# Performance work log

Measured on AMD Instinct MI355X. Metric: run time of the kernel, lower is better.

## Reference

```python
import jax, jax.numpy as jnp
import numpy as np

HID = 512
EMB = 768
TOP_K = 8
LN_EPS = 1e-5
NORM_EPS = 1e-12


def _mlp_ln(x, W1, b1, W2, b2, g, beta):
    # Linear -> ReLU -> Linear -> LayerNorm
    h = jax.nn.relu(x @ W1 + b1)
    h = h @ W2 + b2
    mu = jnp.mean(h, axis=-1, keepdims=True)
    var = jnp.var(h, axis=-1, keepdims=True)
    return (h - mu) * jax.lax.rsqrt(var + LN_EPS) * g + beta


def _l2norm(x):
    n = jnp.linalg.norm(x, axis=-1, keepdims=True)
    return x / jnp.maximum(n, NORM_EPS)


def setup_inputs() -> dict:
    key = jax.random.key(0)
    ks = jax.random.split(key, 12)
    s_in = 1.0 / np.sqrt(EMB)
    s_h = 1.0 / np.sqrt(HID)
    inp = {
        "query_embeddings": jax.random.normal(ks[0], (64, 32, EMB), jnp.float32),
        "doc_embeddings": jax.random.normal(ks[1], (50000, 16, EMB), jnp.float32),
        "qW1": jax.random.normal(ks[2], (EMB, HID), jnp.float32) * s_in,
        "qb1": jnp.zeros((HID,), jnp.float32),
        "qW2": jax.random.normal(ks[3], (HID, HID), jnp.float32) * s_h,
        "qb2": jnp.zeros((HID,), jnp.float32),
        "qg": jnp.ones((HID,), jnp.float32),
        "qbeta": jnp.zeros((HID,), jnp.float32),
        "dW1": jax.random.normal(ks[4], (EMB, HID), jnp.float32) * s_in,
        "db1": jnp.zeros((HID,), jnp.float32),
        "dW2": jax.random.normal(ks[5], (HID, HID), jnp.float32) * s_h,
        "db2": jnp.zeros((HID,), jnp.float32),
        "dg": jnp.ones((HID,), jnp.float32),
        "dbeta": jnp.zeros((HID,), jnp.float32),
        "pW": jax.random.normal(ks[6], (HID, HID), jnp.float32) * s_h,
        "pb": jnp.zeros((HID,), jnp.float32),
        "temperature": jnp.asarray(1.0, jnp.float32),
    }
    return inp


def reference(query_embeddings, doc_embeddings, qW1, qb1, qW2, qb2, qg, qbeta,
              dW1, db1, dW2, db2, dg, dbeta, pW, pb, temperature):
    # Mean-pool over token dims, encode with MLP+LayerNorm
    q_repr = _mlp_ln(query_embeddings.mean(axis=1), qW1, qb1, qW2, qb2, qg, qbeta)  # [B,H]
    d_repr = _mlp_ln(doc_embeddings.mean(axis=1), dW1, db1, dW2, db2, dg, dbeta)    # [N,H]
    q_norm = _l2norm(q_repr @ pW + pb)
    d_norm = _l2norm(d_repr @ pW + pb)
    scores = (q_norm @ d_norm.T) / temperature  # [B,N]
    top_k_scores, top_k_indices = jax.lax.top_k(scores, TOP_K)  # [B,K]
    retrieved_docs = doc_embeddings[top_k_indices]  # [B,K,doc_len,EMB]
    return top_k_scores, retrieved_docs
```

## Files before the change

### kernel.cpp

```cpp
#include <hip/hip_runtime.h>

#define NQ 64
#define ND 50000
#define NDP 50048
#define MT (NDP + NQ)
#define QTOK 32
#define DTOK 16
#define EMB 768
#define HID 512

typedef short s16x8 __attribute__((ext_vector_type(8)));
typedef float f32x4 __attribute__((ext_vector_type(4)));

__device__ __forceinline__ unsigned short f2bf(float f) {
    union { float f; unsigned u; } x; x.f = f;
    unsigned r = x.u + 0x7fffu + ((x.u >> 16) & 1u);
    return (unsigned short)(r >> 16);
}
__device__ __forceinline__ float bf2f(unsigned short h) {
    union { unsigned u; float f; } x; x.u = ((unsigned)h) << 16;
    return x.f;
}
__device__ __forceinline__ unsigned packhi2(float a, float b) {
    return (unsigned)f2bf(a) | ((unsigned)f2bf(b) << 16);
}
__device__ __forceinline__ unsigned packlo2(float a, float b) {
    unsigned short ha = f2bf(a), hb = f2bf(b);
    return (unsigned)f2bf(a - bf2f(ha)) | ((unsigned)f2bf(b - bf2f(hb)) << 16);
}

__device__ __forceinline__ void gload_lds16(const void* g, void* l) {
    __builtin_amdgcn_global_load_lds(
        (const __attribute__((address_space(1))) void*)g,
        (__attribute__((address_space(3))) void*)l, 16, 0, 0);
}


__global__ void pool_aug_all(const float* __restrict__ de, const float* __restrict__ qe,
                             ushort* __restrict__ out) {
    int blk = blockIdx.x, t = threadIdx.x;
    const float* src;
    int T;
    size_t orow;
    if (blk < ND) { src = de + (size_t)blk * DTOK * EMB; T = DTOK; orow = blk; }
    else          { int qr = blk - ND; src = qe + (size_t)qr * QTOK * EMB; T = QTOK; orow = NDP + qr; }
    const float4* ip = (const float4*)src + t;
    float4 a = make_float4(0.f, 0.f, 0.f, 0.f);
    for (int i = 0; i < T; ++i) {
        float4 v = ip[(size_t)i * (EMB / 4)];
        a.x += v.x; a.y += v.y; a.z += v.z; a.w += v.w;
    }
    const float s = 1.0f / (float)T;
    float v0 = a.x * s, v1 = a.y * s, v2 = a.z * s, v3 = a.w * s;
    ushort* base = out + orow * (2 * EMB);
    *(uint2*)(base + t * 4)       = make_uint2(packhi2(v0, v1), packhi2(v2, v3));
    *(uint2*)(base + EMB + t * 4) = make_uint2(packlo2(v0, v1), packlo2(v2, v3));
}

__global__ void wconv_all(const float* __restrict__ dW1, const float* __restrict__ qW1,
                          const float* __restrict__ dW2, const float* __restrict__ qW2,
                          const float* __restrict__ pW,
                          const float* __restrict__ dg, const float* __restrict__ qg,
                          ushort* __restrict__ W1p, ushort* __restrict__ QW1p,
                          ushort* __restrict__ W2p, ushort* __restrict__ QW2p,
                          ushort* __restrict__ W3d, ushort* __restrict__ W3q) {
    int n = blockIdx.x, seg = blockIdx.y;
    const float* W; const float* scale = nullptr; ushort* o; int K;
    switch (seg) {
        case 0:  W = dW1; o = W1p;  K = EMB; break;
        case 1:  W = qW1; o = QW1p; K = EMB; break;
        case 2:  W = dW2; o = W2p;  K = HID; break;
        case 3:  W = qW2; o = QW2p; K = HID; break;
        case 4:  W = pW;  o = W3d;  K = HID; scale = dg; break;
        default: W = pW;  o = W3q;  K = HID; scale = qg; break;
    }
    ushort* base = o + (size_t)n * 2 * K;
    for (int k = threadIdx.x; k < K; k += blockDim.x) {
        float v = W[(size_t)k * HID + n];
        if (scale) v *= scale[k];
        unsigned short hi = f2bf(v);
        base[k]     = hi;
        base[K + k] = f2bf(v - bf2f(hi));
    }
}

__global__ void uv_prep(const float* __restrict__ pW, const float* __restrict__ pb,
                        const float* __restrict__ dg, const float* __restrict__ dbe,
                        const float* __restrict__ qg, const float* __restrict__ qbe,
                        float* __restrict__ ud, float* __restrict__ vvd,
                        float* __restrict__ uq, float* __restrict__ vvq) {
    int n = blockIdx.x;
    float a = 0.f, b = 0.f, c = 0.f, d = 0.f;
    for (int k = threadIdx.x; k < HID; k += 256) {
        float w = pW[(size_t)k * HID + n];
        a += dg[k] * w; b += dbe[k] * w; c += qg[k] * w; d += qbe[k] * w;
    }
    #pragma unroll
    for (int o = 32; o > 0; o >>= 1) {
        a += __shfl_xor(a, o); b += __shfl_xor(b, o);
        c += __shfl_xor(c, o); d += __shfl_xor(d, o);
    }
    __shared__ float red[4][4];
    int wv = threadIdx.x >> 6, ln = threadIdx.x & 63;
    if (ln == 0) { red[wv][0] = a; red[wv][1] = b; red[wv][2] = c; red[wv][3] = d; }
    __syncthreads();
    if (threadIdx.x == 0) {
        float A = 0, B = 0, C = 0, D = 0;
        #pragma unroll
        for (int i = 0; i < 4; ++i) { A += red[i][0]; B += red[i][1]; C += red[i][2]; D += red[i][3]; }
        ud[n] = A; vvd[n] = B + pb[n]; uq[n] = C; vvq[n] = D + pb[n];
    }
}

template <int MODE>
__global__ __launch_bounds__(512, 4) void mfma_gemm2(const ushort* __restrict__ A,
                                                     const ushort* __restrict__ Bd,
                                                     const ushort* __restrict__ Bq,
                                                     const float* __restrict__ pard,
                                                     const float* __restrict__ parq,
                                                     const float* __restrict__ auxd,
                                                     const float* __restrict__ auxq,
                                                     const float2* __restrict__ statsIn,
                                                     float2* __restrict__ sumsOut,
                                                     float* __restrict__ normpOut,
                                                     void* __restrict__ out,
                                                     int M, int K) {
    __shared__ ushort As[128 * 64];
    __shared__ ushort Bs[256 * 64];
    __shared__ float redS[4][128];
    __shared__ float redQ[4][128];
    const int Ks = 2 * K;
    const int bm = blockIdx.x * 128;
    const int bn = blockIdx.y * 256;
    const bool isq = (bm >= NDP);
    const ushort* B = isq ? Bq : Bd;
    const int tid = threadIdx.x;
    const int lane = tid & 63;
    const int wave = tid >> 6;
    const int wr = wave >> 2;
    const int wc = wave & 3;
    f32x4 acc[4][4] = {};

    for (int k0 = 0; k0 < 3 * K; k0 += 64) {
        const int ka = (k0 < 2 * K) ? k0 : k0 - 2 * K;
        const int kb = (k0 < K) ? k0 : k0 - K;
        #pragma unroll
        for (int c = 0; c < 2; ++c) {
            int idx = c * 512 + tid;
            int row = idx >> 3, s = idx & 7;
            int gr = bm + row; if (gr >= M) gr = M - 1;
            int ks = (s ^ (row & 7)) << 3;
            gload_lds16(A + (size_t)gr * Ks + ka + ks, As + idx * 8);
        }
        #pragma unroll
        for (int c = 0; c < 4; ++c) {
            int idx = c * 512 + tid;
            int n = idx >> 3, s = idx & 7;
            int ks = (s ^ (n & 7)) << 3;
            gload_lds16(B + (size_t)(bn + n) * Ks + kb + ks, Bs + idx * 8);
        }
        __syncthreads();

        #pragma unroll
        for (int kk = 0; kk < 2; ++kk) {
            const int sp = kk * 4 + (lane >> 4);
            s16x8 a[4], b[4];
            #pragma unroll
            for (int i = 0; i < 4; ++i) {
                int r = wr * 64 + i * 16 + (lane & 15);
                a[i] = *(const s16x8*)(As + r * 64 + ((sp ^ (r & 7)) << 3));
            }
            #pragma unroll
            for (int j = 0; j < 4; ++j) {
                int n = wc * 64 + j * 16 + (lane & 15);
                b[j] = *(const s16x8*)(Bs + n * 64 + ((sp ^ (n & 7)) << 3));
            }
            #pragma unroll
            for (int i = 0; i < 4; ++i)
                #pragma unroll
                for (int j = 0; j < 4; ++j)
                    acc[i][j] = __builtin_amdgcn_mfma_f32_16x16x32_bf16(a[i], b[j], acc[i][j], 0, 0, 0);
        }
        __syncthreads();
    }

    if (MODE == 1 || MODE == 2) {
        const float* bias = isq ? parq : pard;
        float bv[4];
        #pragma unroll
        for (int j = 0; j < 4; ++j) bv[j] = bias[bn + wc * 64 + j * 16 + (lane & 15)];

        if (MODE == 2) {
            #pragma unroll
            for (int i = 0; i < 4; ++i)
                #pragma unroll
                for (int r = 0; r < 4; ++r) {
                    float ps = 0.f, pq = 0.f;
                    #pragma unroll
                    for (int j = 0; j < 4; ++j) {
                        float v = acc[i][j][r] + bv[j];
                        ps += v; pq += v * v;
                    }
                    #pragma unroll
                    for (int o = 1; o < 16; o <<= 1) { ps += __shfl_xor(ps, o); pq += __shfl_xor(pq, o); }
                    if ((lane & 15) == 0) {
                        int rl = wr * 64 + i * 16 + ((lane >> 4) << 2) + r;
                        redS[wc][rl] = ps; redQ[wc][rl] = pq;
                    }
                }
            __syncthreads();
            if (tid < 128) {
                float s = redS[0][tid] + redS[1][tid] + redS[2][tid] + redS[3][tid];
                float q = redQ[0][tid] + redQ[1][tid] + redQ[2][tid] + redQ[3][tid];
                int grow = bm + tid;
                if (grow < M) sumsOut[(size_t)grow * 2 + blockIdx.y] = make_float2(s, q);
            }
        }

        #pragma unroll
        for (int j = 0; j < 4; ++j) {
            int col = bn + wc * 64 + j * 16 + (lane & 15);
            #pragma unroll
            for (int i = 0; i < 4; ++i)
                #pragma unroll
                for (int r = 0; r < 4; ++r) {
                    int grow = bm + wr * 64 + i * 16 + ((lane >> 4) << 2) + r;
                    if (grow >= M) continue;
                    float v = acc[i][j][r] + bv[j];
                    if (MODE == 1) v = fmaxf(v, 0.0f);
                    unsigned short hi = f2bf(v);
                    ushort* op = (ushort*)out + (size_t)grow * (2 * HID);
                    op[col]       = hi;
                    op[HID + col] = f2bf(v - bf2f(hi));
                }
        }
    } else {
        const float* u  = isq ? parq : pard;
        const float* vv = isq ? auxq : auxd;
        float uj[4], vj[4];
        #pragma unroll
        for (int j = 0; j < 4; ++j) {
            int col = bn + wc * 64 + j * 16 + (lane & 15);
            uj[j] = u[col]; vj[j] = vv[col];
        }
        #pragma unroll
        for (int i = 0; i < 4; ++i)
            #pragma unroll
            for (int r = 0; r < 4; ++r) {
                int grow = bm + wr * 64 + i * 16 + ((lane >> 4) << 2) + r;
                int gsr  = grow < M ? grow : M - 1;
                float2 p0 = statsIn[(size_t)gsr * 2 + 0];
                float2 p1 = statsIn[(size_t)gsr * 2 + 1];
                float s  = p0.x + p1.x, qq = p0.y + p1.y;
                float mu  = s * (1.0f / 512.0f);
                float var = qq * (1.0f / 512.0f) - mu * mu;
                float rs  = rsqrtf(var + 1e-5f);
                float ps = 0.f;
                #pragma unroll
                for (int j = 0; j < 4; ++j) {
                    float val = rs * (acc[i][j][r] - mu * uj[j]) + vj[j];
                    ps += val * val;
                    if (grow < M) {
                        int col = bn + wc * 64 + j * 16 + (lane & 15);
                        unsigned short hi = f2bf(val);
                        ushort* op = (ushort*)out + (size_t)grow * (2 * HID);
                        op[col]       = hi;
                        op[HID + col] = f2bf(val - bf2f(hi));
                    }
                }
                #pragma unroll
                for (int o = 1; o < 16; o <<= 1) ps += __shfl_xor(ps, o);
                if ((lane & 15) == 0) {
                    int rl = wr * 64 + i * 16 + ((lane >> 4) << 2) + r;
                    redS[wc][rl] = ps;
                }
            }
        __syncthreads();
        if (tid < 128) {
            float s = redS[0][tid] + redS[1][tid] + redS[2][tid] + redS[3][tid];
            int grow = bm + tid;
            if (grow < M) normpOut[(size_t)grow * 2 + blockIdx.y] = s;
        }
    }
}

__global__ __launch_bounds__(512, 4) void mfma_scores(const ushort* __restrict__ A,
                                                      const ushort* __restrict__ B,
                                                      const float* __restrict__ normp,
                                                      float* __restrict__ out,
                                                      int M, int N_B, int K, long ldo,
                                                      const float* __restrict__ temp, int rowOff) {
    __shared__ ushort As[128 * 64];
    __shared__ ushort Bs[256 * 64];
    const int Ks = 2 * K;
    const int bm = blockIdx.x * 128;
    const int bn = blockIdx.y * 256;
    const int tid = threadIdx.x;
    const int lane = tid & 63;
    const int wave = tid >> 6;
    const int wr = wave >> 2;
    const int wc = wave & 3;
    f32x4 acc[4][4] = {};

    for (int k0 = 0; k0 < 3 * K; k0 += 64) {
        const int ka = (k0 < 2 * K) ? k0 : k0 - 2 * K;
        const int kb = (k0 < K) ? k0 : k0 - K;
        #pragma unroll
        for (int c = 0; c < 2; ++c) {
            int idx = c * 512 + tid;
            int row = idx >> 3, s = idx & 7;
            int gr = bm + row; if (gr >= M) gr = M - 1;
            int ks = (s ^ (row & 7)) << 3;
            gload_lds16(A + (size_t)gr * Ks + ka + ks, As + idx * 8);
        }
        #pragma unroll
        for (int c = 0; c < 4; ++c) {
            int idx = c * 512 + tid;
            int n = idx >> 3, s = idx & 7;
            int gn = bn + n; if (gn >= N_B) gn = N_B - 1;
            int ks = (s ^ (n & 7)) << 3;
            gload_lds16(B + (size_t)gn * Ks + kb + ks, Bs + idx * 8);
        }
        __syncthreads();

        #pragma unroll
        for (int kk = 0; kk < 2; ++kk) {
            const int sp = kk * 4 + (lane >> 4);
            s16x8 a[4], b[4];
            #pragma unroll
            for (int i = 0; i < 4; ++i) {
                int r = wr * 64 + i * 16 + (lane & 15);
                a[i] = *(const s16x8*)(As + r * 64 + ((sp ^ (r & 7)) << 3));
            }
            #pragma unroll
            for (int j = 0; j < 4; ++j) {
                int n = wc * 64 + j * 16 + (lane & 15);
                b[j] = *(const s16x8*)(Bs + n * 64 + ((sp ^ (n & 7)) << 3));
            }
            #pragma unroll
            for (int i = 0; i < 4; ++i)
                #pragma unroll
                for (int j = 0; j < 4; ++j)
                    acc[i][j] = __builtin_amdgcn_mfma_f32_16x16x32_bf16(a[i], b[j], acc[i][j], 0, 0, 0);
        }
        __syncthreads();
    }

    float invT = 1.0f / temp[0];
    float rB[4];
    #pragma unroll
    for (int j = 0; j < 4; ++j) {
        int gcol = bn + wc * 64 + j * 16 + (lane & 15);
        int gc = gcol < N_B ? gcol : N_B - 1;
        float n2 = normp[(size_t)gc * 2] + normp[(size_t)gc * 2 + 1];
        rB[j] = 1.0f / fmaxf(sqrtf(n2), 1e-12f);
    }
    #pragma unroll
    for (int i = 0; i < 4; ++i)
        #pragma unroll
        for (int r = 0; r < 4; ++r) {
            int grow = bm + wr * 64 + i * 16 + ((lane >> 4) << 2) + r;
            int gr = grow < M ? grow : M - 1;
            float n2a = normp[(size_t)(rowOff + gr) * 2] + normp[(size_t)(rowOff + gr) * 2 + 1];
            float rA = 1.0f / fmaxf(sqrtf(n2a), 1e-12f);
            #pragma unroll
            for (int j = 0; j < 4; ++j) {
                int gcol = bn + wc * 64 + j * 16 + (lane & 15);
                if (grow < M && gcol < N_B)
                    out[(size_t)grow * ldo + gcol] = acc[i][j][r] * rA * rB[j] * invT;
            }
        }
}

__global__ __launch_bounds__(256) void topk_kernel(const float* __restrict__ scores,
                                                   float* __restrict__ out_scores,
                                                   int* __restrict__ out_idx, int N) {
    __shared__ float ls[2048];
    __shared__ int   li[2048];
    const int q   = blockIdx.x;
    const int tid = threadIdx.x;
    const float* row = scores + (size_t)q * N;
    float s[8]; int ix[8];
    #pragma unroll
    for (int i = 0; i < 8; ++i) { s[i] = -1e30f; ix[i] = 0x7fffffff; }
    for (int j = tid; j < N; j += 256) {
        float v = row[j];
        if (v > s[7]) {
            s[7] = v; ix[7] = j;
            #pragma unroll
            for (int t = 7; t > 0; --t) {
                bool sw = (s[t] > s[t-1]) || (s[t] == s[t-1] && ix[t] < ix[t-1]);
                if (sw) {
                    float tv = s[t]; s[t] = s[t-1]; s[t-1] = tv;
                    int   ti = ix[t]; ix[t] = ix[t-1]; ix[t-1] = ti;
                }
            }
        }
    }
    #pragma unroll
    for (int i = 0; i < 8; ++i) { ls[tid * 8 + i] = s[i]; li[tid * 8 + i] = ix[i]; }
    __syncthreads();
    for (int w = 64; w >= 1; w >>= 2) {
        if (tid < w) {
            #pragma unroll
            for (int i = 0; i < 8; ++i) { s[i] = -1e30f; ix[i] = 0x7fffffff; }
            #pragma unroll
            for (int c = 0; c < 32; ++c) {
                float v  = ls[tid * 32 + c];
                int   vi = li[tid * 32 + c];
                bool better = (v > s[7]) || (v == s[7] && vi < ix[7]);
                if (better) {
                    s[7] = v; ix[7] = vi;
                    #pragma unroll
                    for (int t = 7; t > 0; --t) {
                        bool sw = (s[t] > s[t-1]) || (s[t] == s[t-1] && ix[t] < ix[t-1]);
                        if (sw) {
                            float tv = s[t]; s[t] = s[t-1]; s[t-1] = tv;
                            int   ti = ix[t]; ix[t] = ix[t-1]; ix[t-1] = ti;
                        }
                    }
                }
            }
        }
        __syncthreads();
        if (tid < w) {
            #pragma unroll
            for (int i = 0; i < 8; ++i) { ls[tid * 8 + i] = s[i]; li[tid * 8 + i] = ix[i]; }
        }
        __syncthreads();
    }
    if (tid < 8) {
        out_scores[(size_t)q * 8 + tid] = ls[tid];
        out_idx[q * 8 + tid]            = li[tid];
    }
}

__global__ __launch_bounds__(256) void gather_kernel(const float* __restrict__ docs,
                                                     const int* __restrict__ idx,
                                                     float* __restrict__ out) {
    const int b = blockIdx.x;
    const int d = idx[b];
    const float4* src = (const float4*)(docs + (size_t)d * DTOK * EMB);
    float4*       dst = (float4*)(out + (size_t)b * DTOK * EMB);
    for (int i = threadIdx.x; i < DTOK * EMB / 4; i += 256) dst[i] = src[i];
}

extern "C" void kernel_launch(void* const* d_in, const int* in_sizes, int n_in,
                              void* d_out, int out_size, void* d_ws, size_t ws_size,
                              hipStream_t stream) {
    const float* qe   = (const float*)d_in[0];
    const float* de   = (const float*)d_in[1];
    const float* qW1  = (const float*)d_in[2];
    const float* qb1  = (const float*)d_in[3];
    const float* qW2  = (const float*)d_in[4];
    const float* qb2  = (const float*)d_in[5];
    const float* qg   = (const float*)d_in[6];
    const float* qbe  = (const float*)d_in[7];
    const float* dW1  = (const float*)d_in[8];
    const float* db1  = (const float*)d_in[9];
    const float* dW2  = (const float*)d_in[10];
    const float* db2  = (const float*)d_in[11];
    const float* dg   = (const float*)d_in[12];
    const float* dbe  = (const float*)d_in[13];
    const float* pW   = (const float*)d_in[14];
    const float* pb   = (const float*)d_in[15];
    const float* temp = (const float*)d_in[16];

    float* out = (float*)d_out;

    char* w = (char*)d_ws;
    float*  scores = (float*)w;                 w += (size_t)NQ * ND * 4;
    ushort* W1p    = (ushort*)w;                w += (size_t)HID * 2 * EMB * 2;
    ushort* W2p    = (ushort*)w;                w += (size_t)HID * 2 * HID * 2;
    ushort* W3d    = (ushort*)w;                w += (size_t)HID * 2 * HID * 2;
    ushort* QW1p   = (ushort*)w;                w += (size_t)HID * 2 * EMB * 2;
    ushort* QW2p   = (ushort*)w;                w += (size_t)HID * 2 * HID * 2;
    ushort* W3q    = (ushort*)w;                w += (size_t)HID * 2 * HID * 2;
    float*  ud     = (float*)w;                 w += HID * 4;
    float*  vvd    = (float*)w;                 w += HID * 4;
    float*  uq     = (float*)w;                 w += HID * 4;
    float*  vvq    = (float*)w;                 w += HID * 4;
    float2* sums   = (float2*)w;                w += (size_t)MT * 2 * 8;
    float*  normp  = (float*)w;                 w += (size_t)MT * 2 * 4;
    int*    tidx   = (int*)w;                   w += 4096;
    ushort* pooled = (ushort*)w;                w += (size_t)MT * 2 * EMB * 2;
    ushort* h1a    = (ushort*)w;                w += (size_t)MT * 2 * HID * 2;
    ushort* h2a    = pooled;
    ushort* Daug   = h1a;
    ushort* qaug   = Daug + (size_t)NDP * 2 * HID;

    const int GM = (MT + 127) / 128;

    wconv_all<<<dim3(512, 6), 256, 0, stream>>>(dW1, qW1, dW2, qW2, pW, dg, qg,
                                                W1p, QW1p, W2p, QW2p, W3d, W3q);
    uv_prep<<<512, 256, 0, stream>>>(pW, pb, dg, dbe, qg, qbe, ud, vvd, uq, vvq);

    pool_aug_all<<<ND + NQ, 192, 0, stream>>>(de, qe, pooled);
    mfma_gemm2<1><<<dim3(GM, 2), 512, 0, stream>>>(pooled, W1p, QW1p, db1, qb1,
                                                   nullptr, nullptr, nullptr, nullptr, nullptr,
                                                   h1a, MT, EMB);
    mfma_gemm2<2><<<dim3(GM, 2), 512, 0, stream>>>(h1a, W2p, QW2p, db2, qb2,
                                                   nullptr, nullptr, nullptr, sums, nullptr,
                                                   h2a, MT, HID);
    mfma_gemm2<3><<<dim3(GM, 2), 512, 0, stream>>>(h2a, W3d, W3q, ud, uq,
                                                   vvd, vvq, sums, nullptr, normp,
                                                   Daug, MT, HID);

    mfma_scores<<<dim3(1, (ND + 255) / 256), 512, 0, stream>>>(qaug, Daug, normp, scores,
                                                               NQ, ND, HID, (long)ND, temp, NDP);

    topk_kernel<<<NQ, 256, 0, stream>>>(scores, out, tidx, ND);
    gather_kernel<<<NQ * 8, 256, 0, stream>>>(de, tidx, out + NQ * 8);
}
```

Measured before the change: 1.299 ms.

## Triple-buffer LDS tiles with async prefetch in GEMM and scores kernels

Both MFMA GEMM kernels switch from a single LDS buffer with load-then-sync to a three-slot ring. Tiles are prefetched two K-steps ahead, with explicit vmcnt waits and raw s_barriers in place of __syncthreads. The goal is to overlap global-to-LDS transfers with MFMA compute. LDS use triples to about 144 KB per block and the occupancy hint of 4 is dropped, so fewer blocks can be resident per CU.

```diff
diff --git a/kernel.cpp b/kernel.cpp
--- a/kernel.cpp
+++ b/kernel.cpp
@@ -113,20 +113,20 @@
 }
 
 template <int MODE>
-__global__ __launch_bounds__(512, 4) void mfma_gemm2(const ushort* __restrict__ A,
-                                                     const ushort* __restrict__ Bd,
-                                                     const ushort* __restrict__ Bq,
-                                                     const float* __restrict__ pard,
-                                                     const float* __restrict__ parq,
-                                                     const float* __restrict__ auxd,
-                                                     const float* __restrict__ auxq,
-                                                     const float2* __restrict__ statsIn,
-                                                     float2* __restrict__ sumsOut,
-                                                     float* __restrict__ normpOut,
-                                                     void* __restrict__ out,
-                                                     int M, int K) {
-    __shared__ ushort As[128 * 64];
-    __shared__ ushort Bs[256 * 64];
+__global__ __launch_bounds__(512) void mfma_gemm2(const ushort* __restrict__ A,
+                                                  const ushort* __restrict__ Bd,
+                                                  const ushort* __restrict__ Bq,
+                                                  const float* __restrict__ pard,
+                                                  const float* __restrict__ parq,
+                                                  const float* __restrict__ auxd,
+                                                  const float* __restrict__ auxq,
+                                                  const float2* __restrict__ statsIn,
+                                                  float2* __restrict__ sumsOut,
+                                                  float* __restrict__ normpOut,
+                                                  void* __restrict__ out,
+                                                  int M, int K) {
+    __shared__ ushort As[3][128 * 64];
+    __shared__ ushort Bs[3][256 * 64];
     __shared__ float redS[4][128];
     __shared__ float redQ[4][128];
     const int Ks = 2 * K;
@@ -139,28 +139,47 @@
     const int wave = tid >> 6;
     const int wr = wave >> 2;
     const int wc = wave & 3;
+    const int nt = (3 * K) >> 6;
     f32x4 acc[4][4] = {};
 
-    for (int k0 = 0; k0 < 3 * K; k0 += 64) {
+    auto STAGE = [&](int kt, int slot) {
+        const int k0 = kt << 6;
         const int ka = (k0 < 2 * K) ? k0 : k0 - 2 * K;
         const int kb = (k0 < K) ? k0 : k0 - K;
+        ushort* Asl = &As[slot][0];
+        ushort* Bsl = &Bs[slot][0];
         #pragma unroll
         for (int c = 0; c < 2; ++c) {
             int idx = c * 512 + tid;
             int row = idx >> 3, s = idx & 7;
             int gr = bm + row; if (gr >= M) gr = M - 1;
             int ks = (s ^ (row & 7)) << 3;
-            gload_lds16(A + (size_t)gr * Ks + ka + ks, As + idx * 8);
+            gload_lds16(A + (size_t)gr * Ks + ka + ks, Asl + idx * 8);
         }
         #pragma unroll
         for (int c = 0; c < 4; ++c) {
             int idx = c * 512 + tid;
             int n = idx >> 3, s = idx & 7;
             int ks = (s ^ (n & 7)) << 3;
-            gload_lds16(B + (size_t)(bn + n) * Ks + kb + ks, Bs + idx * 8);
-        }
-        __syncthreads();
-
+            gload_lds16(B + (size_t)(bn + n) * Ks + kb + ks, Bsl + idx * 8);
+        }
+    };
+
+    STAGE(0, 0);
+    STAGE(1, 1);
+    for (int t = 0; t < nt; ++t) {
+        if (t + 2 < nt) {
+            STAGE(t + 2, (t + 2) % 3);
+            asm volatile("s_waitcnt vmcnt(12)" ::: "memory");
+        } else if (t + 1 < nt) {
+            asm volatile("s_waitcnt vmcnt(6)" ::: "memory");
+        } else {
+            asm volatile("s_waitcnt vmcnt(0)" ::: "memory");
+        }
+        __builtin_amdgcn_sched_barrier(0);
+        __builtin_amdgcn_s_barrier();
+        const ushort* Asl = &As[t % 3][0];
+        const ushort* Bsl = &Bs[t % 3][0];
         #pragma unroll
         for (int kk = 0; kk < 2; ++kk) {
             const int sp = kk * 4 + (lane >> 4);
@@ -168,12 +187,12 @@
             #pragma unroll
             for (int i = 0; i < 4; ++i) {
                 int r = wr * 64 + i * 16 + (lane & 15);
-                a[i] = *(const s16x8*)(As + r * 64 + ((sp ^ (r & 7)) << 3));
+                a[i] = *(const s16x8*)(Asl + r * 64 + ((sp ^ (r & 7)) << 3));
             }
             #pragma unroll
             for (int j = 0; j < 4; ++j) {
                 int n = wc * 64 + j * 16 + (lane & 15);
-                b[j] = *(const s16x8*)(Bs + n * 64 + ((sp ^ (n & 7)) << 3));
+                b[j] = *(const s16x8*)(Bsl + n * 64 + ((sp ^ (n & 7)) << 3));
             }
             #pragma unroll
             for (int i = 0; i < 4; ++i)
@@ -181,7 +200,8 @@
                 for (int j = 0; j < 4; ++j)
                     acc[i][j] = __builtin_amdgcn_mfma_f32_16x16x32_bf16(a[i], b[j], acc[i][j], 0, 0, 0);
         }
-        __syncthreads();
+        __builtin_amdgcn_sched_barrier(0);
+        __builtin_amdgcn_s_barrier();
     }
 
     if (MODE == 1 || MODE == 2) {
@@ -284,14 +304,14 @@
     }
 }
 
-__global__ __launch_bounds__(512, 4) void mfma_scores(const ushort* __restrict__ A,
-                                                      const ushort* __restrict__ B,
-                                                      const float* __restrict__ normp,
-                                                      float* __restrict__ out,
-                                                      int M, int N_B, int K, long ldo,
-                                                      const float* __restrict__ temp, int rowOff) {
-    __shared__ ushort As[128 * 64];
-    __shared__ ushort Bs[256 * 64];
+__global__ __launch_bounds__(512) void mfma_scores(const ushort* __restrict__ A,
+                                                   const ushort* __restrict__ B,
+                                                   const float* __restrict__ normp,
+                                                   float* __restrict__ out,
+                                                   int M, int N_B, int K, long ldo,
+                                                   const float* __restrict__ temp, int rowOff) {
+    __shared__ ushort As[3][128 * 64];
+    __shared__ ushort Bs[3][256 * 64];
     const int Ks = 2 * K;
     const int bm = blockIdx.x * 128;
     const int bn = blockIdx.y * 256;
@@ -300,18 +320,22 @@
     const int wave = tid >> 6;
     const int wr = wave >> 2;
     const int wc = wave & 3;
+    const int nt = (3 * K) >> 6;
     f32x4 acc[4][4] = {};
 
-    for (int k0 = 0; k0 < 3 * K; k0 += 64) {
+    auto STAGE = [&](int kt, int slot) {
+        const int k0 = kt << 6;
         const int ka = (k0 < 2 * K) ? k0 : k0 - 2 * K;
         const int kb = (k0 < K) ? k0 : k0 - K;
+        ushort* Asl = &As[slot][0];
+        ushort* Bsl = &Bs[slot][0];
         #pragma unroll
         for (int c = 0; c < 2; ++c) {
             int idx = c * 512 + tid;
             int row = idx >> 3, s = idx & 7;
             int gr = bm + row; if (gr >= M) gr = M - 1;
             int ks = (s ^ (row & 7)) << 3;
-            gload_lds16(A + (size_t)gr * Ks + ka + ks, As + idx * 8);
+            gload_lds16(A + (size_t)gr * Ks + ka + ks, Asl + idx * 8);
         }
         #pragma unroll
         for (int c = 0; c < 4; ++c) {
@@ -319,10 +343,25 @@
             int n = idx >> 3, s = idx & 7;
             int gn = bn + n; if (gn >= N_B) gn = N_B - 1;
             int ks = (s ^ (n & 7)) << 3;
-            gload_lds16(B + (size_t)gn * Ks + kb + ks, Bs + idx * 8);
-        }
-        __syncthreads();
-
+            gload_lds16(B + (size_t)gn * Ks + kb + ks, Bsl + idx * 8);
+        }
+    };
+
+    STAGE(0, 0);
+    STAGE(1, 1);
+    for (int t = 0; t < nt; ++t) {
+        if (t + 2 < nt) {
+            STAGE(t + 2, (t + 2) % 3);
+            asm volatile("s_waitcnt vmcnt(12)" ::: "memory");
+        } else if (t + 1 < nt) {
+            asm volatile("s_waitcnt vmcnt(6)" ::: "memory");
+        } else {
+            asm volatile("s_waitcnt vmcnt(0)" ::: "memory");
+        }
+        __builtin_amdgcn_sched_barrier(0);
+        __builtin_amdgcn_s_barrier();
+        const ushort* Asl = &As[t % 3][0];
+        const ushort* Bsl = &Bs[t % 3][0];
         #pragma unroll
         for (int kk = 0; kk < 2; ++kk) {
             const int sp = kk * 4 + (lane >> 4);
@@ -330,12 +369,12 @@
             #pragma unroll
             for (int i = 0; i < 4; ++i) {
                 int r = wr * 64 + i * 16 + (lane & 15);
-                a[i] = *(const s16x8*)(As + r * 64 + ((sp ^ (r & 7)) << 3));
+                a[i] = *(const s16x8*)(Asl + r * 64 + ((sp ^ (r & 7)) << 3));
             }
             #pragma unroll
             for (int j = 0; j < 4; ++j) {
                 int n = wc * 64 + j * 16 + (lane & 15);
-                b[j] = *(const s16x8*)(Bs + n * 64 + ((sp ^ (n & 7)) << 3));
+                b[j] = *(const s16x8*)(Bsl + n * 64 + ((sp ^ (n & 7)) << 3));
             }
             #pragma unroll
             for (int i = 0; i < 4; ++i)
@@ -343,7 +382,8 @@
                 for (int j = 0; j < 4; ++j)
                     acc[i][j] = __builtin_amdgcn_mfma_f32_16x16x32_bf16(a[i], b[j], acc[i][j], 0, 0, 0);
         }
-        __syncthreads();
+        __builtin_amdgcn_sched_barrier(0);
+        __builtin_amdgcn_s_barrier();
     }
 
     float invT = 1.0f / temp[0];
```

After: 1.474 ms. +13.4%, slower.
